# Optimization experiments

Hardware: AMD Instinct MI355X
Metric: run time of the kernel (lower is better)

The kernel has to match this reference:

```python
import jax, jax.numpy as jnp
import numpy as np

B, S, D = 4, 1024, 768
H = 12
E = 4
DF = 3072
TOPK = 2
# expert domain map: language->0 (LINGUISTIC), logic->1 (SYMBOLIC), spatial->0, causal->1
DOMAIN_MAP = jnp.array([0, 1, 0, 1], dtype=jnp.int32)


def layernorm(x, g, b, eps=1e-5):
    mu = jnp.mean(x, axis=-1, keepdims=True)
    var = jnp.mean(jnp.square(x - mu), axis=-1, keepdims=True)
    return (x - mu) * jax.lax.rsqrt(var + eps) * g + b


def setup_inputs() -> dict:
    key = jax.random.key(0)
    ks = jax.random.split(key, 10)
    sc = 0.02
    return {
        "x": jax.random.normal(ks[0], (B, S, D), jnp.float32),
        "ln1_g": jnp.ones((D,), jnp.float32),
        "ln1_b": jnp.zeros((D,), jnp.float32),
        "Wq": jax.random.normal(ks[1], (D, D), jnp.float32) * sc,
        "Wk": jax.random.normal(ks[2], (D, D), jnp.float32) * sc,
        "Wv": jax.random.normal(ks[3], (D, D), jnp.float32) * sc,
        "Wo": jax.random.normal(ks[4], (D, D), jnp.float32) * sc,
        "Wt": jax.random.normal(ks[5], (D, 2), jnp.float32) * sc,
        "bt": jnp.zeros((2,), jnp.float32),
        "ln2_g": jnp.ones((D,), jnp.float32),
        "ln2_b": jnp.zeros((D,), jnp.float32),
        "Wg": jax.random.normal(ks[6], (D, E), jnp.float32) * sc,
        "W1": jax.random.normal(ks[7], (E, D, DF), jnp.float32) * sc,
        "b1": jnp.zeros((E, DF), jnp.float32),
        "W2": jax.random.normal(ks[8], (E, DF, D), jnp.float32) * sc,
        "b2": jnp.zeros((E, D), jnp.float32),
    }


def reference(x, ln1_g, ln1_b, Wq, Wk, Wv, Wo, Wt, bt, ln2_g, ln2_b, Wg, W1, b1, W2, b2):
    hd = D // H
    # --- task-conditioned routing bias ---
    pooled = jnp.mean(x, axis=1)                      # [B, D]
    task_logits = pooled @ Wt + bt                    # [B, 2]
    routing_bias = task_logits[:, DOMAIN_MAP]         # [B, E]
    # --- multi-head self-attention with pre-norm residual ---
    h = layernorm(x, ln1_g, ln1_b)
    q = (h @ Wq).reshape(B, S, H, hd)
    k = (h @ Wk).reshape(B, S, H, hd)
    v = (h @ Wv).reshape(B, S, H, hd)
    scores = jnp.einsum("bqhd,bkhd->bhqk", q, k) / jnp.sqrt(jnp.float32(hd))
    attn = jax.nn.softmax(scores, axis=-1)
    ctx = jnp.einsum("bhqk,bkhd->bqhd", attn, v).reshape(B, S, D)
    x = x + ctx @ Wo
    # --- top-k MoE with routing bias, pre-norm residual ---
    h2 = layernorm(x, ln2_g, ln2_b)
    gate_logits = h2 @ Wg + routing_bias[:, None, :]  # [B, S, E]
    topv, topi = jax.lax.top_k(gate_logits, TOPK)     # [B, S, k]
    w = jax.nn.softmax(topv, axis=-1)                 # renormalized top-k weights
    gates = jnp.sum(jax.nn.one_hot(topi, E, dtype=x.dtype) * w[..., None], axis=-2)  # [B,S,E]
    hid = jax.nn.gelu(jnp.einsum("bsd,edf->bsef", h2, W1) + b1)       # [B,S,E,DF]
    y = jnp.einsum("bsef,efd->bsed", hid, W2) + b2                    # [B,S,E,D]
    moe_out = jnp.einsum("bsed,bse->bsd", y, gates)
    return x + moe_out
```

## Files before the change

### kernel.cpp

```cpp
#include <hip/hip_runtime.h>
#include <hip/hip_bf16.h>

using bf16 = __hip_bfloat16;
typedef float f32x4 __attribute__((ext_vector_type(4)));
typedef short bf16x8 __attribute__((ext_vector_type(8)));

#define DD 768
#define SS 1024
#define HH 12
#define DFF 3072

__device__ __forceinline__ float bf2f(bf16 v) { return __bfloat162float(v); }
__device__ __forceinline__ bf16 f2bf(float v) { return __float2bfloat16(v); }
__device__ __forceinline__ float sb2f(short u) {
  return __uint_as_float(((unsigned)(unsigned short)u) << 16);
}
__device__ __forceinline__ short f2sb(float f) {
  bf16 b = f2bf(f);
  return reinterpret_cast<short&>(b);
}

__device__ __forceinline__ void gld16(const void* g, void* l) {
  __builtin_amdgcn_global_load_lds(
      (const __attribute__((address_space(1))) void*)g,
      (__attribute__((address_space(3))) void*)l, 16, 0, 0);
}

__global__ __launch_bounds__(256) void transpose_cast_kernel(
    const float* __restrict__ src, bf16* __restrict__ dst,
    int R, int C, long sstride, long dstride)
{
  __shared__ float tile[64][65];
  const int c0 = blockIdx.x * 64, r0 = blockIdx.y * 64;
  const float* s = src + (long)blockIdx.z * sstride + (long)r0 * C + c0;
  bf16* d = dst + (long)blockIdx.z * dstride + (long)c0 * R + r0;
  const int rr = threadIdx.x >> 4;
  const int cc = (threadIdx.x & 15) * 4;
  #pragma unroll
  for (int k = 0; k < 4; k++) {
    const f32x4 v = *(const f32x4*)(s + (long)(rr + k * 16) * C + cc);
    *(f32x4*)(&tile[rr + k * 16][cc]) = v;
  }
  __syncthreads();
  #pragma unroll
  for (int k = 0; k < 4; k++) {
    const int c = rr + k * 16;
    short4 pk = make_short4(f2sb(tile[cc + 0][c]), f2sb(tile[cc + 1][c]),
                            f2sb(tile[cc + 2][c]), f2sb(tile[cc + 3][c]));
    *(short4*)(d + (long)c * R + cc) = pk;
  }
}

__global__ __launch_bounds__(256) void transpose4_kernel(
    const float* __restrict__ s0, const float* __restrict__ s1,
    const float* __restrict__ s2, const float* __restrict__ s3,
    bf16* __restrict__ dst)
{
  __shared__ float tile[64][65];
  const int z = blockIdx.z;
  const float* src = (z == 0) ? s0 : (z == 1) ? s1 : (z == 2) ? s2 : s3;
  const int c0 = blockIdx.x * 64, r0 = blockIdx.y * 64;
  const float* s = src + (long)r0 * 768 + c0;
  bf16* d = dst + (long)z * 589824 + (long)c0 * 768 + r0;
  const int rr = threadIdx.x >> 4;
  const int cc = (threadIdx.x & 15) * 4;
  #pragma unroll
  for (int k = 0; k < 4; k++) {
    const f32x4 v = *(const f32x4*)(s + (long)(rr + k * 16) * 768 + cc);
    *(f32x4*)(&tile[rr + k * 16][cc]) = v;
  }
  __syncthreads();
  #pragma unroll
  for (int k = 0; k < 4; k++) {
    const int c = rr + k * 16;
    short4 pk = make_short4(f2sb(tile[cc + 0][c]), f2sb(tile[cc + 1][c]),
                            f2sb(tile[cc + 2][c]), f2sb(tile[cc + 3][c]));
    *(short4*)(d + (long)c * 768 + cc) = pk;
  }
}

__global__ __launch_bounds__(256) void ln1pool_kernel(
    const float* __restrict__ x, const float* __restrict__ g,
    const float* __restrict__ b, bf16* __restrict__ out,
    float* __restrict__ pp)
{
  __shared__ float buf[4][768];
  const int w = threadIdx.x >> 6, lane = threadIdx.x & 63;
  const int row = blockIdx.x * 4 + w;
  const float* xr = x + (long)row * DD;
  float v[12];
  float s = 0.f;
  #pragma unroll
  for (int i = 0; i < 12; i++) { v[i] = xr[lane + i * 64]; s += v[i]; }
  #pragma unroll
  for (int o = 1; o < 64; o <<= 1) s += __shfl_xor(s, o, 64);
  const float mu = s * (1.f / DD);
  float vs = 0.f;
  #pragma unroll
  for (int i = 0; i < 12; i++) { const float d = v[i] - mu; vs += d * d; }
  #pragma unroll
  for (int o = 1; o < 64; o <<= 1) vs += __shfl_xor(vs, o, 64);
  const float rstd = rsqrtf(vs * (1.f / DD) + 1e-5f);
  bf16* orow = out + (long)row * DD;
  #pragma unroll
  for (int i = 0; i < 12; i++) {
    const int d = lane + i * 64;
    orow[d] = f2bf((v[i] - mu) * rstd * g[d] + b[d]);
    buf[w][d] = v[i];
  }
  __syncthreads();
  for (int c = threadIdx.x; c < 768; c += 256)
    pp[(long)blockIdx.x * 768 + c] = buf[0][c] + buf[1][c] + buf[2][c] + buf[3][c];
}

__global__ __launch_bounds__(256) void pool2_kernel(
    const float* __restrict__ pp, float* __restrict__ pooled)
{
  const int idx = blockIdx.x * 256 + threadIdx.x;
  const int bb = idx / 768, d = idx % 768;
  const float* p = pp + (long)bb * 256 * 768 + d;
  float s = 0.f;
  for (int c = 0; c < 256; c++) s += p[(long)c * 768];
  pooled[idx] = s * (1.f / SS);
}

__global__ __launch_bounds__(256) void route_kernel(
    const float* __restrict__ pooled, const float* __restrict__ Wt,
    const float* __restrict__ bt, float* __restrict__ rbias)
{
  __shared__ float tl[8];
  const int pair = threadIdx.x >> 5, l = threadIdx.x & 31;
  const int b = pair >> 1, j = pair & 1;
  float s = 0.f;
  for (int i = l; i < DD; i += 32) s += pooled[b * DD + i] * Wt[i * 2 + j];
  #pragma unroll
  for (int o = 1; o < 32; o <<= 1) s += __shfl_xor(s, o, 64);
  if (l == 0) tl[pair] = s + bt[j];
  __syncthreads();
  if (threadIdx.x < 16) {
    const int bb = threadIdx.x >> 2, e = threadIdx.x & 3;
    rbias[threadIdx.x] = tl[bb * 2 + (e & 1)];
  }
}

__device__ __forceinline__ float gelu_tanh(float x) {
  const float u = 0.7978845608028654f * (x + 0.044715f * x * x * x);
  const float e = __expf(2.f * u);
  const float t = 1.f - 2.f / (e + 1.f);
  return 0.5f * x * (1.f + t);
}

template <int MODE>
__global__ __launch_bounds__(256) void gemm128_kernel(
    const bf16* __restrict__ A, const bf16* __restrict__ Bt,
    bf16* __restrict__ Cbf, float* __restrict__ Cf,
    int N, int K, int NT, int GX,
    const float* __restrict__ aux1, const float* __restrict__ gates,
    const int* __restrict__ tokl, const int* __restrict__ cnt_es,
    bf16* __restrict__ yB)
{
  __shared__ __align__(16) bf16 As[2][128 * 32];
  __shared__ __align__(16) bf16 Bs[2][128 * 32];

  const int nwg = gridDim.x;
  const int orig = blockIdx.x;
  const int q = nwg >> 3, r = nwg & 7;
  const int xcd = orig & 7, sidx = orig >> 3;
  const int wgid = (xcd < r ? xcd * (q + 1) : r * (q + 1) + (xcd - r) * q) + sidx;

  const int n0 = (wgid % GX) * 128;
  int m0 = 0, e = 0, g0 = 0, row0 = 0, nval = 0x7fffffff, kseg = 0, kh = 0;
  if (MODE >= 2) {
    int p = wgid / GX;
    if (MODE == 3) { kh = p & 1; p >>= 1; }
    int sacc = 0, pacc = 0, found = 0;
    #pragma unroll
    for (int k = 0; k < 8; k++) {
      const int c = cnt_es[k];
      const int pk = (c + 127) >> 7;
      if (!found && p < pacc + pk) {
        found = 1; kseg = k; e = k & 3;
        g0 = (p - pacc) * 128; row0 = sacc + g0; nval = c;
      }
      pacc += pk; sacc += c;
    }
    if (!found) return;
  } else {
    m0 = (wgid / GX) * 128;
  }
  const int kofs = (MODE == 3) ? kh * 1536 : 0;

  const int tid = threadIdx.x;
  const int lane = tid & 63, wv = tid >> 6;
  const int wr = wv >> 1, wc = wv & 1;
  const int lrow = lane & 15, lk = lane >> 4;
  const int lr = lrow, lg = lk;
  const int srow = lane >> 2;
  const int csw = (((lane & 3) ^ ((srow >> 1) & 3)) * 8);

  const bf16* Be = (MODE >= 2) ? Bt + (long)e * N * K : Bt;
  const bf16* arow[2];
  const bf16* brow[2];
  #pragma unroll
  for (int u = 0; u < 2; u++) {
    const int rbr = u * 64 + wv * 16 + srow;
    if (MODE == 2) {
      const int g = g0 + rbr;
      const int tk = (g < nval) ? tokl[kseg * 4096 + g] : tokl[kseg * 4096];
      arow[u] = A + (long)tk * K;
    } else if (MODE == 3) {
      int rr = row0 + rbr; if (rr > 8191) rr = 8191;
      arow[u] = A + (long)rr * K + kofs;
    } else {
      arow[u] = A + (long)(m0 + rbr) * K;
    }
    brow[u] = Be + (long)(n0 + rbr) * K + kofs;
  }

  f32x4 acc[4][4] = {};

#define STAGE(T, BUF)                                                   \
  {                                                                     \
    const int k0s = (T) * 32;                                           \
    _Pragma("unroll")                                                   \
    for (int u = 0; u < 2; u++) {                                       \
      const int rb = u * 64 + wv * 16;                                  \
      gld16(arow[u] + k0s + csw, &As[BUF][rb * 32]);                    \
      gld16(brow[u] + k0s + csw, &Bs[BUF][rb * 32]);                    \
    }                                                                   \
  }

  STAGE(0, 0)
  __syncthreads();

  for (int t = 0; t < NT; t++) {
    const int buf = t & 1;
    if (t + 1 < NT) STAGE(t + 1, buf ^ 1)

    bf16x8 af[4], bfr[4];
    #pragma unroll
    for (int i = 0; i < 4; i++) {
      const int ra = wr * 64 + i * 16 + lrow;
      const int rbw = wc * 64 + i * 16 + lrow;
      af[i]  = *(const bf16x8*)(&As[buf][ra * 32 + ((lk ^ ((ra >> 1) & 3)) * 8)]);
      bfr[i] = *(const bf16x8*)(&Bs[buf][rbw * 32 + ((lk ^ ((rbw >> 1) & 3)) * 8)]);
    }
    #pragma unroll
    for (int i = 0; i < 4; i++)
      #pragma unroll
      for (int j = 0; j < 4; j++)
        acc[i][j] = __builtin_amdgcn_mfma_f32_16x16x32_bf16(bfr[j], af[i], acc[i][j], 0, 0, 0);
    __syncthreads();
  }
#undef STAGE

  #pragma unroll
  for (int i = 0; i < 4; i++) {
    const int rloc = wr * 64 + i * 16 + lr;
    #pragma unroll
    for (int j = 0; j < 4; j++) {
      const int col = n0 + wc * 64 + j * 16 + lg * 4;
      const f32x4 v = acc[i][j];
      if (MODE == 0) {
        const long row = m0 + rloc;
        short4 pk = make_short4(f2sb(v[0]), f2sb(v[1]), f2sb(v[2]), f2sb(v[3]));
        *(short4*)(&Cbf[row * N + col]) = pk;
      } else if (MODE == 1) {
        const long idx = (long)(m0 + rloc) * N + col;
        const f32x4 xv = *(const f32x4*)(&aux1[idx]);
        f32x4 o = xv + v;
        *(f32x4*)(&Cf[idx]) = o;
      } else if (MODE == 2) {
        const int g = g0 + rloc;
        if (g < nval) {
          const float* b1e = aux1 + (long)e * N;
          const f32x4 bb = *(const f32x4*)(&b1e[col]);
          short4 pk = make_short4(f2sb(gelu_tanh(v[0] + bb[0])),
                                  f2sb(gelu_tanh(v[1] + bb[1])),
                                  f2sb(gelu_tanh(v[2] + bb[2])),
                                  f2sb(gelu_tanh(v[3] + bb[3])));
          *(short4*)(&Cbf[(long)(row0 - g0 + g) * N + col]) = pk;
        }
      } else {
        const int g = g0 + rloc;
        if (g < nval) {
          const int tk = tokl[kseg * 4096 + g];
          const float gt = gates[tk * 4 + e];
          f32x4 vb = v;
          if (kh == 0) {
            const float* b2e = aux1 + (long)e * N;
            const f32x4 bb = *(const f32x4*)(&b2e[col]);
            vb = v + bb;
          }
          const int pidx = (kseg >> 2) * 2 + kh;
          bf16* yp = (pidx < 3) ? Cbf + (long)pidx * 3145728 : yB;
          short4 pk = make_short4(f2sb(gt * vb[0]), f2sb(gt * vb[1]),
                                  f2sb(gt * vb[2]), f2sb(gt * vb[3]));
          *(short4*)(&yp[(long)tk * 768 + col]) = pk;
        }
      }
    }
  }
}

__global__ __launch_bounds__(256) void fuse_kernel(
    const bf16* __restrict__ yA, const bf16* __restrict__ yB,
    float* __restrict__ out)
{
  const long i = ((long)blockIdx.x * 256 + threadIdx.x) * 4;
  const short4 a = *(const short4*)((const short*)yA + i);
  const short4 b = *(const short4*)((const short*)yA + 3145728 + i);
  const short4 c = *(const short4*)((const short*)yA + 6291456 + i);
  const short4 d = *(const short4*)((const short*)yB + i);
  f32x4 o = *(f32x4*)(&out[i]);
  o[0] += sb2f(a.x) + sb2f(b.x) + sb2f(c.x) + sb2f(d.x);
  o[1] += sb2f(a.y) + sb2f(b.y) + sb2f(c.y) + sb2f(d.y);
  o[2] += sb2f(a.z) + sb2f(b.z) + sb2f(c.z) + sb2f(d.z);
  o[3] += sb2f(a.w) + sb2f(b.w) + sb2f(c.w) + sb2f(d.w);
  *(f32x4*)(&out[i]) = o;
}

__global__ __launch_bounds__(256) void vtrans_kernel(
    const bf16* __restrict__ qkv, bf16* __restrict__ vt)
{
  __shared__ short t[64][72];
  const int kt = blockIdx.x;
  const int bh = blockIdx.y;
  const int b = bh / HH, h = bh % HH;
  const int tid = threadIdx.x;
  const short* vg = (const short*)qkv + ((long)(b * SS + kt * 64)) * 2304 + 1536 + h * 64;
  #pragma unroll
  for (int i = 0; i < 2; i++) {
    const int idx = i * 256 + tid;
    const int r = idx >> 3, c = (idx & 7) * 8;
    *(bf16x8*)(&t[r][c]) = *(const bf16x8*)(vg + (long)r * 2304 + c);
  }
  __syncthreads();
  short* vo = (short*)vt + (long)bh * 64 * SS + kt * 64;
  #pragma unroll
  for (int i = 0; i < 2; i++) {
    const int idx = i * 256 + tid;
    const int d = idx >> 3, r0 = (idx & 7) * 8;
    bf16x8 o;
    #pragma unroll
    for (int j = 0; j < 8; j++) o[j] = t[r0 + j][d];
    *(bf16x8*)(vo + (long)d * SS + r0) = o;
  }
}

__global__ __launch_bounds__(256) void attn_kernel(
    const bf16* __restrict__ qkv, const bf16* __restrict__ vt,
    bf16* __restrict__ ctx)
{
  __shared__ __align__(16) short Qs[64 * 64];
  __shared__ __align__(16) short Ks[64 * 64];
  __shared__ __align__(16) short Vts[64 * 64];
  __shared__ __align__(16) short Ps[4][16 * 64];

  const int qt = blockIdx.x;
  const int bh = blockIdx.y;
  const int b = bh / HH, h = bh % HH;
  const int tid = threadIdx.x, lane = tid & 63, w = tid >> 6;
  const int lr = lane & 15, lg = lane >> 4;

  const short* qg = (const short*)qkv + ((long)(b * SS + qt * 64)) * 2304 + h * 64;
  #pragma unroll
  for (int i = 0; i < 2; i++) {
    const int idx = i * 256 + tid;
    const int r = idx >> 3, c8 = idx & 7;
    bf16x8 v = *(const bf16x8*)(qg + (long)r * 2304 + c8 * 8);
    bf16x8 o;
    #pragma unroll
    for (int j = 0; j < 8; j++) o[j] = f2sb(sb2f(v[j]) * 0.125f);
    *(bf16x8*)(&Qs[r * 64 + ((c8 ^ (r & 7)) * 8)]) = o;
  }
  __syncthreads();

  bf16x8 aq[2];
  {
    const int r = w * 16 + lr;
    aq[0] = *(const bf16x8*)(&Qs[r * 64 + (((lg + 0) ^ (r & 7)) * 8)]);
    aq[1] = *(const bf16x8*)(&Qs[r * 64 + (((lg + 4) ^ (r & 7)) * 8)]);
  }

  float m_run[4], l_run[4];
  f32x4 oacc[4];
  #pragma unroll
  for (int r = 0; r < 4; r++) { m_run[r] = -1e30f; l_run[r] = 0.f; }
  #pragma unroll
  for (int dt = 0; dt < 4; dt++) oacc[dt] = (f32x4){0.f, 0.f, 0.f, 0.f};

  const short* kg = (const short*)qkv + ((long)(b * SS)) * 2304 + 768 + h * 64;
  const short* vg = (const short*)vt + ((long)bh * 64) * SS;
  const int sr = lane >> 3, sc = lane & 7;

  for (int kt = 0; kt < 16; kt++) {
    __syncthreads();
    #pragma unroll
    for (int c = 0; c < 2; c++) {
      const int rb = c * 32 + w * 8;
      const int row = rb + sr;
      const int ch = sc ^ (row & 7);
      gld16(kg + ((long)(kt * 64 + row)) * 2304 + ch * 8, &Ks[rb * 64]);
      gld16(vg + ((long)row) * SS + kt * 64 + ch * 8, &Vts[rb * 64]);
    }
    __syncthreads();

    f32x4 s[4];
    #pragma unroll
    for (int jt = 0; jt < 4; jt++) {
      const int r = jt * 16 + lr;
      bf16x8 bk0 = *(const bf16x8*)(&Ks[r * 64 + (((lg + 0) ^ (r & 7)) * 8)]);
      bf16x8 bk1 = *(const bf16x8*)(&Ks[r * 64 + (((lg + 4) ^ (r & 7)) * 8)]);
      f32x4 a = {};
      a = __builtin_amdgcn_mfma_f32_16x16x32_bf16(aq[0], bk0, a, 0, 0, 0);
      a = __builtin_amdgcn_mfma_f32_16x16x32_bf16(aq[1], bk1, a, 0, 0, 0);
      s[jt] = a;
    }

    #pragma unroll
    for (int r = 0; r < 4; r++) {
      float mt = fmaxf(fmaxf(s[0][r], s[1][r]), fmaxf(s[2][r], s[3][r]));
      mt = fmaxf(mt, __shfl_xor(mt, 1, 64));
      mt = fmaxf(mt, __shfl_xor(mt, 2, 64));
      mt = fmaxf(mt, __shfl_xor(mt, 4, 64));
      mt = fmaxf(mt, __shfl_xor(mt, 8, 64));
      const float mn = fmaxf(m_run[r], mt);
      const float sc0 = __expf(m_run[r] - mn);
      m_run[r] = mn;
      float p0 = __expf(s[0][r] - mn), p1 = __expf(s[1][r] - mn);
      float p2 = __expf(s[2][r] - mn), p3 = __expf(s[3][r] - mn);
      float rs = p0 + p1 + p2 + p3;
      rs += __shfl_xor(rs, 1, 64);
      rs += __shfl_xor(rs, 2, 64);
      rs += __shfl_xor(rs, 4, 64);
      rs += __shfl_xor(rs, 8, 64);
      l_run[r] = l_run[r] * sc0 + rs;
      #pragma unroll
      for (int dt = 0; dt < 4; dt++) oacc[dt][r] *= sc0;
      const int prow = lg * 4 + r;
      const int pswz = (prow & 7) << 3;
      Ps[w][prow * 64 + ((0 * 16 + lr) ^ pswz)] = f2sb(p0);
      Ps[w][prow * 64 + ((1 * 16 + lr) ^ pswz)] = f2sb(p1);
      Ps[w][prow * 64 + ((2 * 16 + lr) ^ pswz)] = f2sb(p2);
      Ps[w][prow * 64 + ((3 * 16 + lr) ^ pswz)] = f2sb(p3);
    }

    bf16x8 pa0 = *(const bf16x8*)(&Ps[w][lr * 64 + (((lg + 0) ^ (lr & 7)) << 3)]);
    bf16x8 pa1 = *(const bf16x8*)(&Ps[w][lr * 64 + (((lg + 4) ^ (lr & 7)) << 3)]);
    #pragma unroll
    for (int dt = 0; dt < 4; dt++) {
      const int r = dt * 16 + lr;
      bf16x8 bv0 = *(const bf16x8*)(&Vts[r * 64 + (((lg + 0) ^ (r & 7)) * 8)]);
      bf16x8 bv1 = *(const bf16x8*)(&Vts[r * 64 + (((lg + 4) ^ (r & 7)) * 8)]);
      oacc[dt] = __builtin_amdgcn_mfma_f32_16x16x32_bf16(pa0, bv0, oacc[dt], 0, 0, 0);
      oacc[dt] = __builtin_amdgcn_mfma_f32_16x16x32_bf16(pa1, bv1, oacc[dt], 0, 0, 0);
    }
  }

  #pragma unroll
  for (int r = 0; r < 4; r++) {
    const float inv = 1.f / l_run[r];
    const long row = (long)(b * SS + qt * 64 + w * 16 + lg * 4 + r);
    #pragma unroll
    for (int dt = 0; dt < 4; dt++)
      ctx[row * DD + h * 64 + dt * 16 + lr] = f2bf(oacc[dt][r] * inv);
  }
}

__global__ __launch_bounds__(256) void lngate_kernel(
    const float* __restrict__ x2, const float* __restrict__ g,
    const float* __restrict__ bln, const float* __restrict__ Wg,
    const float* __restrict__ rbias, bf16* __restrict__ h2,
    float* __restrict__ gates)
{
  const int t = blockIdx.x * 4 + (threadIdx.x >> 6);
  const int lane = threadIdx.x & 63;
  const int b = t >> 10;
  const float* xr = x2 + (long)t * DD;
  float v[12];
  float s = 0.f;
  #pragma unroll
  for (int i = 0; i < 12; i++) { v[i] = xr[lane + i * 64]; s += v[i]; }
  #pragma unroll
  for (int o = 1; o < 64; o <<= 1) s += __shfl_xor(s, o, 64);
  const float mu = s * (1.f / DD);
  float vs = 0.f;
  #pragma unroll
  for (int i = 0; i < 12; i++) { const float d = v[i] - mu; vs += d * d; }
  #pragma unroll
  for (int o = 1; o < 64; o <<= 1) vs += __shfl_xor(vs, o, 64);
  const float rstd = rsqrtf(vs * (1.f / DD) + 1e-5f);
  bf16* orow = h2 + (long)t * DD;
  float a0 = 0.f, a1 = 0.f, a2 = 0.f, a3 = 0.f;
  #pragma unroll
  for (int i = 0; i < 12; i++) {
    const int d = lane + i * 64;
    const float hv = (v[i] - mu) * rstd * g[d] + bln[d];
    orow[d] = f2bf(hv);
    const f32x4 w = *(const f32x4*)(&Wg[d * 4]);
    a0 += hv * w.x; a1 += hv * w.y; a2 += hv * w.z; a3 += hv * w.w;
  }
  #pragma unroll
  for (int o = 1; o < 64; o <<= 1) {
    a0 += __shfl_xor(a0, o, 64); a1 += __shfl_xor(a1, o, 64);
    a2 += __shfl_xor(a2, o, 64); a3 += __shfl_xor(a3, o, 64);
  }
  if (lane == 0) {
    float lg4[4] = { a0 + rbias[b * 4 + 0], a1 + rbias[b * 4 + 1],
                     a2 + rbias[b * 4 + 2], a3 + rbias[b * 4 + 3] };
    int i1 = 0;
    #pragma unroll
    for (int e = 1; e < 4; e++) if (lg4[e] > lg4[i1]) i1 = e;
    int i2 = -1;
    #pragma unroll
    for (int e = 0; e < 4; e++) if (e != i1 && (i2 < 0 || lg4[e] > lg4[i2])) i2 = e;
    const float e2 = __expf(lg4[i2] - lg4[i1]);
    const float den = 1.f + e2;
    float og[4] = {0.f, 0.f, 0.f, 0.f};
    og[i1] = 1.f / den;
    og[i2] = e2 / den;
    *(f32x4*)(&gates[t * 4]) = (f32x4){og[0], og[1], og[2], og[3]};
  }
}

__global__ __launch_bounds__(1024) void compact_kernel(
    const float* __restrict__ gates, int* __restrict__ tokl,
    int* __restrict__ cnt)
{
  __shared__ int wtot[8][16];
  const int tid = threadIdx.x;
  const int lane = tid & 63, w = tid >> 6;
  int sA[4], sB[4];
  int lc[8] = {0, 0, 0, 0, 0, 0, 0, 0};
  #pragma unroll
  for (int i = 0; i < 4; i++) {
    const int t = tid * 4 + i;
    const f32x4 g = *(const f32x4*)(&gates[t * 4]);
    int e1 = -1, e2 = -1;
    #pragma unroll
    for (int e = 0; e < 4; e++)
      if (g[e] > 0.f) { if (e1 < 0) e1 = e; else e2 = e; }
    sA[i] = e1; sB[i] = 4 + e2;
    lc[e1]++; lc[4 + e2]++;
  }
  int base[8];
  #pragma unroll
  for (int k = 0; k < 8; k++) {
    int v = lc[k];
    #pragma unroll
    for (int o = 1; o < 64; o <<= 1) {
      const int u = __shfl_up(v, o, 64);
      if (lane >= o) v += u;
    }
    base[k] = v - lc[k];
    if (lane == 63) wtot[k][w] = v;
  }
  __syncthreads();
  #pragma unroll
  for (int k = 0; k < 8; k++) {
    int b = 0;
    for (int ww = 0; ww < 16; ww++)
      if (ww < w) b += wtot[k][ww];
    base[k] += b;
  }
  #pragma unroll
  for (int i = 0; i < 4; i++) {
    const int t = tid * 4 + i;
    tokl[sA[i] * 4096 + base[sA[i]]] = t; base[sA[i]]++;
    tokl[sB[i] * 4096 + base[sB[i]]] = t; base[sB[i]]++;
  }
  if (tid < 8) {
    int s = 0;
    for (int ww = 0; ww < 16; ww++) s += wtot[tid][ww];
    cnt[tid] = s;
  }
}

extern "C" void kernel_launch(void* const* d_in, const int* in_sizes, int n_in,
                              void* d_out, int out_size, void* d_ws, size_t ws_size,
                              hipStream_t stream)
{
  (void)in_sizes; (void)n_in; (void)out_size; (void)ws_size;
  const float* x    = (const float*)d_in[0];
  const float* ln1g = (const float*)d_in[1];
  const float* ln1b = (const float*)d_in[2];
  const float* Wq   = (const float*)d_in[3];
  const float* Wk   = (const float*)d_in[4];
  const float* Wv   = (const float*)d_in[5];
  const float* Wo   = (const float*)d_in[6];
  const float* Wt   = (const float*)d_in[7];
  const float* bt   = (const float*)d_in[8];
  const float* ln2g = (const float*)d_in[9];
  const float* ln2b = (const float*)d_in[10];
  const float* Wg   = (const float*)d_in[11];
  const float* W1   = (const float*)d_in[12];
  const float* b1   = (const float*)d_in[13];
  const float* W2   = (const float*)d_in[14];
  const float* b2   = (const float*)d_in[15];
  float* out = (float*)d_out;

  char* ws = (char*)d_ws;
  bf16*  w1t    = (bf16*)(ws + 0);
  bf16*  w2t    = (bf16*)(ws + 18874368);
  bf16*  h2     = (bf16*)(ws + 37748736);
  float* gates  = (float*)(ws + 44040192);
  int*   tokl   = (int*)(ws + 44105728);
  int*   cnt    = (int*)(ws + 44236800);
  float* pooled = (float*)(ws + 44237056);
  float* rbias  = (float*)(ws + 44249344);
  bf16*  wqkv_t = (bf16*)(ws + 44249600);
  bf16*  h1     = (bf16*)(ws + 48968192);
  bf16*  qkv    = (bf16*)(ws + 55259648);
  bf16*  ctx    = (bf16*)(ws + 74134016);
  bf16*  hid    = (bf16*)(ws + 44249600);
  bf16*  wo_t   = wqkv_t + 3 * 589824;
  bf16*  vt     = h1;
  bf16*  yA     = w1t;
  bf16*  yB     = h2;
  float* pp     = (float*)qkv;

  transpose4_kernel<<<dim3(12, 12, 4), 256, 0, stream>>>(Wq, Wk, Wv, Wo, wqkv_t);
  transpose_cast_kernel<<<dim3(48, 12, 4), 256, 0, stream>>>(W1, w1t, 768, 3072, 2359296, 2359296);
  transpose_cast_kernel<<<dim3(12, 48, 4), 256, 0, stream>>>(W2, w2t, 3072, 768, 2359296, 2359296);

  ln1pool_kernel<<<1024, 256, 0, stream>>>(x, ln1g, ln1b, h1, pp);
  pool2_kernel<<<12, 256, 0, stream>>>(pp, pooled);
  route_kernel<<<1, 256, 0, stream>>>(pooled, Wt, bt, rbias);

  gemm128_kernel<0><<<32 * 18, 256, 0, stream>>>(h1, wqkv_t, qkv, nullptr,
                                                 2304, 768, 24, 18,
                                                 nullptr, nullptr, nullptr, nullptr, nullptr);
  vtrans_kernel<<<dim3(16, 48), 256, 0, stream>>>(qkv, vt);
  attn_kernel<<<dim3(16, 48), 256, 0, stream>>>(qkv, vt, ctx);
  gemm128_kernel<1><<<32 * 6, 256, 0, stream>>>(ctx, wo_t, nullptr, out,
                                                768, 768, 24, 6,
                                                x, nullptr, nullptr, nullptr, nullptr);
  lngate_kernel<<<1024, 256, 0, stream>>>(out, ln2g, ln2b, Wg, rbias, h2, gates);
  compact_kernel<<<1, 1024, 0, stream>>>(gates, tokl, cnt);

  gemm128_kernel<2><<<72 * 24, 256, 0, stream>>>(h2, w1t, hid, nullptr,
                                                 3072, 768, 24, 24,
                                                 b1, nullptr, tokl, cnt, nullptr);
  gemm128_kernel<3><<<72 * 2 * 6, 256, 0, stream>>>(hid, w2t, yA, nullptr,
                                                    768, 3072, 48, 6,
                                                    b2, gates, tokl, cnt, yB);
  fuse_kernel<<<3072, 256, 0, stream>>>(yA, yB, out);
}
```

Measured before the change: 332.3 us.

## Use 256x256 tiles with 512 threads for the MoE expert GEMMs

Adds a new gemm256s kernel that handles the routed MoE up- and down-projection GEMMs with 256x256 output tiles and 8 waves per workgroup. Each wave now computes 128x64 of output. The existing 128-tile kernel is trimmed back to the dense QKV and output-projection GEMMs. Larger tiles give more reuse per LDS load and cut the global traffic for weights and gathered activations. In exchange they double LDS per block and raise register pressure (32 accumulators per wave), and they waste more rows on padding in partially filled per-expert segments.

```diff
diff --git a/kernel.cpp b/kernel.cpp
--- a/kernel.cpp
+++ b/kernel.cpp
@@ -155,9 +155,7 @@
     const bf16* __restrict__ A, const bf16* __restrict__ Bt,
     bf16* __restrict__ Cbf, float* __restrict__ Cf,
     int N, int K, int NT, int GX,
-    const float* __restrict__ aux1, const float* __restrict__ gates,
-    const int* __restrict__ tokl, const int* __restrict__ cnt_es,
-    bf16* __restrict__ yB)
+    const float* __restrict__ aux1)
 {
   __shared__ __align__(16) bf16 As[2][128 * 32];
   __shared__ __align__(16) bf16 Bs[2][128 * 32];
@@ -169,26 +167,7 @@
   const int wgid = (xcd < r ? xcd * (q + 1) : r * (q + 1) + (xcd - r) * q) + sidx;
 
   const int n0 = (wgid % GX) * 128;
-  int m0 = 0, e = 0, g0 = 0, row0 = 0, nval = 0x7fffffff, kseg = 0, kh = 0;
-  if (MODE >= 2) {
-    int p = wgid / GX;
-    if (MODE == 3) { kh = p & 1; p >>= 1; }
-    int sacc = 0, pacc = 0, found = 0;
-    #pragma unroll
-    for (int k = 0; k < 8; k++) {
-      const int c = cnt_es[k];
-      const int pk = (c + 127) >> 7;
-      if (!found && p < pacc + pk) {
-        found = 1; kseg = k; e = k & 3;
-        g0 = (p - pacc) * 128; row0 = sacc + g0; nval = c;
-      }
-      pacc += pk; sacc += c;
-    }
-    if (!found) return;
-  } else {
-    m0 = (wgid / GX) * 128;
-  }
-  const int kofs = (MODE == 3) ? kh * 1536 : 0;
+  const int m0 = (wgid / GX) * 128;
 
   const int tid = threadIdx.x;
   const int lane = tid & 63, wv = tid >> 6;
@@ -198,23 +177,13 @@
   const int srow = lane >> 2;
   const int csw = (((lane & 3) ^ ((srow >> 1) & 3)) * 8);
 
-  const bf16* Be = (MODE >= 2) ? Bt + (long)e * N * K : Bt;
   const bf16* arow[2];
   const bf16* brow[2];
   #pragma unroll
   for (int u = 0; u < 2; u++) {
     const int rbr = u * 64 + wv * 16 + srow;
-    if (MODE == 2) {
-      const int g = g0 + rbr;
-      const int tk = (g < nval) ? tokl[kseg * 4096 + g] : tokl[kseg * 4096];
-      arow[u] = A + (long)tk * K;
-    } else if (MODE == 3) {
-      int rr = row0 + rbr; if (rr > 8191) rr = 8191;
-      arow[u] = A + (long)rr * K + kofs;
-    } else {
-      arow[u] = A + (long)(m0 + rbr) * K;
-    }
-    brow[u] = Be + (long)(n0 + rbr) * K + kofs;
+    arow[u] = A + (long)(m0 + rbr) * K;
+    brow[u] = Bt + (long)(n0 + rbr) * K;
   }
 
   f32x4 acc[4][4] = {};
@@ -265,14 +234,128 @@
         const long row = m0 + rloc;
         short4 pk = make_short4(f2sb(v[0]), f2sb(v[1]), f2sb(v[2]), f2sb(v[3]));
         *(short4*)(&Cbf[row * N + col]) = pk;
-      } else if (MODE == 1) {
+      } else {
         const long idx = (long)(m0 + rloc) * N + col;
         const f32x4 xv = *(const f32x4*)(&aux1[idx]);
         f32x4 o = xv + v;
         *(f32x4*)(&Cf[idx]) = o;
-      } else if (MODE == 2) {
-        const int g = g0 + rloc;
-        if (g < nval) {
+      }
+    }
+  }
+}
+
+template <int MODE>
+__global__ __launch_bounds__(512, 2) void gemm256s_kernel(
+    const bf16* __restrict__ A, const bf16* __restrict__ Bt,
+    bf16* __restrict__ Cbf,
+    int N, int K, int NT, int GX,
+    const float* __restrict__ aux1, const float* __restrict__ gates,
+    const int* __restrict__ tokl, const int* __restrict__ cnt_es,
+    bf16* __restrict__ yB)
+{
+  __shared__ __align__(16) bf16 As[2][256 * 32];
+  __shared__ __align__(16) bf16 Bs[2][256 * 32];
+
+  const int nwg = gridDim.x;
+  const int orig = blockIdx.x;
+  const int q = nwg >> 3, r = nwg & 7;
+  const int xcd = orig & 7, sidx = orig >> 3;
+  const int wgid = (xcd < r ? xcd * (q + 1) : r * (q + 1) + (xcd - r) * q) + sidx;
+
+  const int n0 = (wgid % GX) * 256;
+  int e = 0, g0 = 0, row0 = 0, nval = 0, kseg = 0, kh = 0;
+  {
+    int p = wgid / GX;
+    if (MODE == 3) { kh = p & 1; p >>= 1; }
+    int sacc = 0, pacc = 0, found = 0;
+    #pragma unroll
+    for (int k = 0; k < 8; k++) {
+      const int c = cnt_es[k];
+      const int pk = (c + 255) >> 8;
+      if (!found && p < pacc + pk) {
+        found = 1; kseg = k; e = k & 3;
+        g0 = (p - pacc) * 256; row0 = sacc + g0; nval = c;
+      }
+      pacc += pk; sacc += c;
+    }
+    if (!found) return;
+  }
+  const int kofs = (MODE == 3) ? kh * 1536 : 0;
+
+  const int tid = threadIdx.x;
+  const int lane = tid & 63, wv = tid >> 6;
+  const int wr = wv >> 2, wc = wv & 3;
+  const int lrow = lane & 15, lk = lane >> 4;
+  const int lr = lrow, lg = lk;
+  const int srow = lane >> 2;
+  const int csw = (((lane & 3) ^ ((srow >> 1) & 3)) * 8);
+
+  const bf16* Be = Bt + (long)e * N * K;
+  const bf16* arow[2];
+  const bf16* brow[2];
+  #pragma unroll
+  for (int u = 0; u < 2; u++) {
+    const int rbr = u * 128 + wv * 16 + srow;
+    if (MODE == 2) {
+      const int g = g0 + rbr;
+      const int tk = (g < nval) ? tokl[kseg * 4096 + g] : tokl[kseg * 4096];
+      arow[u] = A + (long)tk * K;
+    } else {
+      int rr = row0 + rbr; if (rr > 8191) rr = 8191;
+      arow[u] = A + (long)rr * K + kofs;
+    }
+    brow[u] = Be + (long)(n0 + rbr) * K + kofs;
+  }
+
+  f32x4 acc[8][4] = {};
+
+#define STAGE(T, BUF)                                                   \
+  {                                                                     \
+    const int k0s = (T) * 32;                                           \
+    _Pragma("unroll")                                                   \
+    for (int u = 0; u < 2; u++) {                                       \
+      const int rb = u * 128 + wv * 16;                                 \
+      gld16(arow[u] + k0s + csw, &As[BUF][rb * 32]);                    \
+      gld16(brow[u] + k0s + csw, &Bs[BUF][rb * 32]);                    \
+    }                                                                   \
+  }
+
+  STAGE(0, 0)
+  __syncthreads();
+
+  for (int t = 0; t < NT; t++) {
+    const int buf = t & 1;
+    if (t + 1 < NT) STAGE(t + 1, buf ^ 1)
+
+    bf16x8 af[8], bfr[4];
+    #pragma unroll
+    for (int j = 0; j < 4; j++) {
+      const int rbw = wc * 64 + j * 16 + lrow;
+      bfr[j] = *(const bf16x8*)(&Bs[buf][rbw * 32 + ((lk ^ ((rbw >> 1) & 3)) * 8)]);
+    }
+    #pragma unroll
+    for (int i = 0; i < 8; i++) {
+      const int ra = wr * 128 + i * 16 + lrow;
+      af[i] = *(const bf16x8*)(&As[buf][ra * 32 + ((lk ^ ((ra >> 1) & 3)) * 8)]);
+    }
+    #pragma unroll
+    for (int i = 0; i < 8; i++)
+      #pragma unroll
+      for (int j = 0; j < 4; j++)
+        acc[i][j] = __builtin_amdgcn_mfma_f32_16x16x32_bf16(bfr[j], af[i], acc[i][j], 0, 0, 0);
+    __syncthreads();
+  }
+#undef STAGE
+
+  #pragma unroll
+  for (int i = 0; i < 8; i++) {
+    const int g = g0 + wr * 128 + i * 16 + lr;
+    if (g < nval) {
+      #pragma unroll
+      for (int j = 0; j < 4; j++) {
+        const int col = n0 + wc * 64 + j * 16 + lg * 4;
+        const f32x4 v = acc[i][j];
+        if (MODE == 2) {
           const float* b1e = aux1 + (long)e * N;
           const f32x4 bb = *(const f32x4*)(&b1e[col]);
           short4 pk = make_short4(f2sb(gelu_tanh(v[0] + bb[0])),
@@ -280,10 +363,7 @@
                                   f2sb(gelu_tanh(v[2] + bb[2])),
                                   f2sb(gelu_tanh(v[3] + bb[3])));
           *(short4*)(&Cbf[(long)(row0 - g0 + g) * N + col]) = pk;
-        }
-      } else {
-        const int g = g0 + rloc;
-        if (g < nval) {
+        } else {
           const int tk = tokl[kseg * 4096 + g];
           const float gt = gates[tk * 4 + e];
           f32x4 vb = v;
@@ -629,21 +709,19 @@
   route_kernel<<<1, 256, 0, stream>>>(pooled, Wt, bt, rbias);
 
   gemm128_kernel<0><<<32 * 18, 256, 0, stream>>>(h1, wqkv_t, qkv, nullptr,
-                                                 2304, 768, 24, 18,
-                                                 nullptr, nullptr, nullptr, nullptr, nullptr);
+                                                 2304, 768, 24, 18, nullptr);
   vtrans_kernel<<<dim3(16, 48), 256, 0, stream>>>(qkv, vt);
   attn_kernel<<<dim3(16, 48), 256, 0, stream>>>(qkv, vt, ctx);
   gemm128_kernel<1><<<32 * 6, 256, 0, stream>>>(ctx, wo_t, nullptr, out,
-                                                768, 768, 24, 6,
-                                                x, nullptr, nullptr, nullptr, nullptr);
+                                                768, 768, 24, 6, x);
   lngate_kernel<<<1024, 256, 0, stream>>>(out, ln2g, ln2b, Wg, rbias, h2, gates);
   compact_kernel<<<1, 1024, 0, stream>>>(gates, tokl, cnt);
 
-  gemm128_kernel<2><<<72 * 24, 256, 0, stream>>>(h2, w1t, hid, nullptr,
-                                                 3072, 768, 24, 24,
-                                                 b1, nullptr, tokl, cnt, nullptr);
-  gemm128_kernel<3><<<72 * 2 * 6, 256, 0, stream>>>(hid, w2t, yA, nullptr,
-                                                    768, 3072, 48, 6,
-                                                    b2, gates, tokl, cnt, yB);
+  gemm256s_kernel<2><<<40 * 12, 512, 0, stream>>>(h2, w1t, hid,
+                                                  3072, 768, 24, 12,
+                                                  b1, nullptr, tokl, cnt, nullptr);
+  gemm256s_kernel<3><<<40 * 2 * 3, 512, 0, stream>>>(hid, w2t, yA,
+                                                     768, 3072, 48, 3,
+                                                     b2, gates, tokl, cnt, yB);
   fuse_kernel<<<3072, 256, 0, stream>>>(yA, yB, out);
 }
```

Result: faster. 322.6 us (-2.9%).
